# Performance work log

Hardware: AMD Instinct MI355X
Metric: run time of the kernel (lower is better)

## Reference

```python
import jax, jax.numpy as jnp
import numpy as np

N, D, H, E = 4_194_304, 8, 16, 2  # tokens, d_model, d_hidden, num_expert


def setup_inputs() -> dict:
    key = jax.random.key(0)
    ks = jax.random.split(key, 11)
    def w(k, shape, fan_in):
        return (jax.random.normal(k, shape, jnp.float32) / np.sqrt(fan_in)).astype(jnp.float32)
    return {
        "inp": jax.random.normal(ks[0], (N, D), jnp.float32),
        # non-MoE MLP: Linear(8,16) -> ReLU -> Linear(16,8)
        "W_a": w(ks[1], (D, H), D), "b_a": jnp.zeros((H,), jnp.float32),
        "W_b": w(ks[2], (H, D), H), "b_b": jnp.zeros((D,), jnp.float32),
        # NaiveGate: Linear(d_model, num_expert)
        "Wg": w(ks[3], (D, E), D), "bg": jnp.zeros((E,), jnp.float32),
        # per-expert MLP weights: d_model -> d_hidden -> d_model
        "We1": w(ks[4], (E, D, H), D), "be1": jnp.zeros((E, H), jnp.float32),
        "We2": w(ks[5], (E, H, D), H), "be2": jnp.zeros((E, D), jnp.float32),
    }


def reference(inp, W_a, b_a, W_b, b_b, Wg, bg, We1, be1, We2, be2):
    # non-MoE block: Linear -> ReLU -> Linear
    x = jnp.maximum(inp @ W_a + b_a, 0.0) @ W_b + b_b            # [N, D]
    # NaiveGate, top_k=1: argmax expert; softmax over a single score == 1.0
    logits = x @ Wg + bg                                         # [N, E]
    idx = jnp.argmax(logits, axis=-1)                            # [N]
    onehot = jax.nn.one_hot(idx, logits.shape[-1], dtype=x.dtype)  # [N, E]
    # expert MLPs computed densely for all E=2 experts, then top-1 select
    h = jax.nn.gelu(jnp.einsum('nd,edh->neh', x, We1) + be1, approximate=False)  # [N, E, H]
    y = jnp.einsum('neh,ehd->ned', h, We2) + be2                 # [N, E, D]
    out = jnp.einsum('ned,ne->nd', y, onehot)                    # [N, D]
    return jnp.sum(out)
```

## Files before the change

### kernel.cpp

```cpp
#include <hip/hip_runtime.h>
#include <math.h>

#define BLOCKS  4096
#define THREADS 256
#define NWAVES  (BLOCKS * THREADS / 64)
#define STEP    (NWAVES * 64)

typedef __attribute__((ext_vector_type(8))) short bf16x8;
typedef __attribute__((ext_vector_type(4))) float f32x4;
typedef __attribute__((ext_vector_type(2))) int   iv2;

union BF8 { unsigned u[4]; bf16x8 v; };

__device__ __forceinline__ unsigned cvt_pk_bf16(float lo, float hi)
{
    unsigned r;
    asm("v_cvt_pk_bf16_f32 %0, %1, %2" : "=v"(r) : "v"(lo), "v"(hi));
    return r;
}

__device__ __forceinline__ float gelu_fast(float x)
{
    const float e = __expf(-1.702f * x);
    return x * __builtin_amdgcn_rcpf(1.0f + e);
}

__global__ void moe_prep(const float* __restrict__ Wb,  const float* __restrict__ bb,
                         const float* __restrict__ Wg,  const float* __restrict__ bg,
                         const float* __restrict__ We1, const float* __restrict__ be1,
                         const float* __restrict__ We2, const float* __restrict__ be2,
                         float* __restrict__ wsc)
{
    const int t = threadIdx.x;
    if (t < 16) {
        float s = 0.f;
        #pragma unroll
        for (int d = 0; d < 8; ++d)
            s += Wb[t * 8 + d] * (Wg[d * 2 + 1] - Wg[d * 2 + 0]);
        wsc[t] = s;
    }
    if (t == 16) {
        float s = bg[1] - bg[0];
        #pragma unroll
        for (int d = 0; d < 8; ++d) s += bb[d] * (Wg[d * 2 + 1] - Wg[d * 2 + 0]);
        wsc[16] = s;
    }
    if (t == 17 || t == 18) {
        const int e = t - 17;
        float s = 0.f;
        #pragma unroll
        for (int d = 0; d < 8; ++d) s += be2[e * 8 + d];
        wsc[t] = s;
    }
    if (t >= 32 && t < 64) {
        const int e = (t - 32) >> 4, h = t & 15;
        float s = be1[e * 16 + h];
        #pragma unroll
        for (int d = 0; d < 8; ++d) s += bb[d] * We1[e * 128 + d * 16 + h];
        wsc[t] = s;
    }
    if (t >= 64 && t < 96) {
        const int e = (t - 64) >> 4, h = t & 15;
        float s = 0.f;
        #pragma unroll
        for (int d = 0; d < 8; ++d) s += We2[(e * 16 + h) * 8 + d];
        wsc[t] = s;
    }
    if (t >= 128 && t < 640) {
        const int idx = t - 128;
        const int e = idx >> 8, f = (idx >> 4) & 15, h = idx & 15;
        float s = 0.f;
        #pragma unroll
        for (int d = 0; d < 8; ++d) s += Wb[f * 8 + d] * We1[e * 128 + d * 16 + h];
        wsc[128 + idx] = s;
    }
}

__global__ void __launch_bounds__(THREADS, 4)
moe_main(const float* __restrict__ inp,
         const float* __restrict__ Wa, const float* __restrict__ ba,
         const float* __restrict__ wsc,
         float* __restrict__ blocksums, int ntok)
{
    __shared__ float wavered[4];
    const int t  = threadIdx.x;
    const int l  = t & 63;
    const int lg = l >> 4;
    const int lr = l & 15;
    const bool lo16 = (l < 16);
    const bool lo32 = (l < 32);

    BF8 aWa, aM0, aM1;
    #pragma unroll
    for (int j2 = 0; j2 < 4; ++j2) {
        const float w0 = lo16 ? Wa[(2 * j2) * 16 + lr]     : 0.f;
        const float w1 = lo16 ? Wa[(2 * j2 + 1) * 16 + lr] : 0.f;
        aWa.u[j2] = cvt_pk_bf16(w0, w1);
        const int f0 = 8 * lg + 2 * j2;
        const float m00 = lo32 ? wsc[128 + f0 * 16 + lr]       : 0.f;
        const float m01 = lo32 ? wsc[128 + (f0 + 1) * 16 + lr] : 0.f;
        aM0.u[j2] = cvt_pk_bf16(m00, m01);
        const float m10 = lo32 ? wsc[384 + f0 * 16 + lr]       : 0.f;
        const float m11 = lo32 ? wsc[384 + (f0 + 1) * 16 + lr] : 0.f;
        aM1.u[j2] = cvt_pk_bf16(m10, m11);
    }

    f32x4 cba, ccb0, ccb1, vwg, vs20, vs21;
    #pragma unroll
    for (int r = 0; r < 4; ++r) {
        const int h = lg * 4 + r;
        cba[r]  = ba[h];
        vwg[r]  = wsc[h];
        ccb0[r] = wsc[32 + h];
        ccb1[r] = wsc[48 + h];
        vs20[r] = wsc[64 + h];
        vs21[r] = wsc[80 + h];
    }
    const float cg4  = wsc[16] * 0.25f;
    const float sbq0 = wsc[17] * 0.25f;
    const float sbq1 = wsc[18] * 0.25f;

    int addrB[4];
    #pragma unroll
    for (int j = 0; j < 4; ++j)
        addrB[j] = ((lg * 2 + (j >> 1)) * 16 + lr) * 4;

    const int gwave = (blockIdx.x * THREADS + t) >> 6;
    const float4* __restrict__ p4 = (const float4*)inp;
    float local = 0.f;

    const int niter = ntok / STEP;
    int tok = gwave * 64 + l;
    float4 a0 = p4[2 * tok];
    float4 a1 = p4[2 * tok + 1];

    for (int it = 0; it < niter; ++it) {
        const float4 c0 = a0;
        const float4 c1 = a1;
        if (it + 1 < niter) {
            a0 = p4[2 * (tok + STEP)];
            a1 = p4[2 * (tok + STEP) + 1];
        }
        tok += STEP;

        unsigned pin[4];
        pin[0] = cvt_pk_bf16(c0.x, c0.y);
        pin[1] = cvt_pk_bf16(c0.z, c0.w);
        pin[2] = cvt_pk_bf16(c1.x, c1.y);
        pin[3] = cvt_pk_bf16(c1.z, c1.w);

        #pragma unroll
        for (int m = 0; m < 4; ++m) {
            const int srcA = m * 64 + lr * 4;
            BF8 bin;
            #pragma unroll
            for (int j = 0; j < 4; ++j)
                bin.u[j] = (unsigned)__builtin_amdgcn_ds_bpermute(srcA, (int)pin[j]);

            const f32x4 C = __builtin_amdgcn_mfma_f32_16x16x32_bf16(
                                aWa.v, bin.v, cba, 0, 0, 0);
            f32x4 rh;
            #pragma unroll
            for (int r = 0; r < 4; ++r) rh[r] = fmaxf(C[r], 0.f);

            float pg = cg4;
            #pragma unroll
            for (int r = 0; r < 4; ++r) pg = fmaf(rh[r], vwg[r], pg);
            const iv2 gs = __builtin_amdgcn_permlane32_swap(
                               __float_as_int(pg), __float_as_int(pg),
                               false, false);
            float pg32 = __int_as_float(gs.x) + __int_as_float(gs.y);
            pg32 += __shfl_xor(pg32, 16);
            const bool sel = pg32 > 0.f;

            const unsigned pr0 = cvt_pk_bf16(rh[0], rh[1]);
            const unsigned pr1 = cvt_pk_bf16(rh[2], rh[3]);
            BF8 bb2;
            #pragma unroll
            for (int j = 0; j < 4; ++j)
                bb2.u[j] = (unsigned)__builtin_amdgcn_ds_bpermute(
                               addrB[j], (int)((j & 1) ? pr1 : pr0));

            const f32x4 C0 = __builtin_amdgcn_mfma_f32_16x16x32_bf16(
                                 aM0.v, bb2.v, ccb0, 0, 0, 0);
            const f32x4 C1 = __builtin_amdgcn_mfma_f32_16x16x32_bf16(
                                 aM1.v, bb2.v, ccb1, 0, 0, 0);

            #pragma unroll
            for (int r = 0; r < 4; ++r) {
                const float pre = sel ? C1[r] : C0[r];
                const float g   = gelu_fast(pre);
                const float s2  = sel ? vs21[r] : vs20[r];
                local = fmaf(g, s2, local);
            }
            local += sel ? sbq1 : sbq0;
        }
    }

    #pragma unroll
    for (int off = 32; off > 0; off >>= 1)
        local += __shfl_down(local, off);
    if ((t & 63) == 0) wavered[t >> 6] = local;
    __syncthreads();
    if (t == 0)
        blocksums[blockIdx.x] = wavered[0] + wavered[1] + wavered[2] + wavered[3];
}

__global__ void __launch_bounds__(256)
moe_reduce(const float* __restrict__ blocksums, float* __restrict__ out)
{
    __shared__ float wavered[4];
    float v = 0.f;
    for (int i = threadIdx.x; i < BLOCKS; i += 256) v += blocksums[i];
    #pragma unroll
    for (int off = 32; off > 0; off >>= 1)
        v += __shfl_down(v, off);
    if ((threadIdx.x & 63) == 0) wavered[threadIdx.x >> 6] = v;
    __syncthreads();
    if (threadIdx.x == 0)
        out[0] = wavered[0] + wavered[1] + wavered[2] + wavered[3];
}

extern "C" void kernel_launch(void* const* d_in, const int* in_sizes, int n_in,
                              void* d_out, int out_size, void* d_ws, size_t ws_size,
                              hipStream_t stream)
{
    const float* inp = (const float*)d_in[0];
    const float* Wa  = (const float*)d_in[1];
    const float* ba  = (const float*)d_in[2];
    const float* Wb  = (const float*)d_in[3];
    const float* bb  = (const float*)d_in[4];
    const float* Wg  = (const float*)d_in[5];
    const float* bg  = (const float*)d_in[6];
    const float* We1 = (const float*)d_in[7];
    const float* be1 = (const float*)d_in[8];
    const float* We2 = (const float*)d_in[9];
    const float* be2 = (const float*)d_in[10];

    const int ntok = in_sizes[0] / 8;

    float* wsc       = (float*)d_ws;
    float* blocksums = (float*)d_ws + 640;
    float* out       = (float*)d_out;

    hipLaunchKernelGGL(moe_prep, dim3(1), dim3(640), 0, stream,
                       Wb, bb, Wg, bg, We1, be1, We2, be2, wsc);
    hipLaunchKernelGGL(moe_main, dim3(BLOCKS), dim3(THREADS), 0, stream,
                       inp, Wa, ba, wsc, blocksums, ntok);
    hipLaunchKernelGGL(moe_reduce, dim3(1), dim3(256), 0, stream,
                       blocksums, out);
}
```

Before: 56.37 us.

## Replace grid-stride prefetch loop with one token per thread over larger grid

Launches four times as many blocks so each thread processes a single token, removing the grid-stride loop and its register double-buffered prefetch. This aims to rely on hardware wave scheduling for latency hiding instead of explicit prefetch. In exchange, every block repeats the weight/constant setup, the final reduction kernel sums more partials, and the kernel now assumes the token count equals the grid size exactly.

```diff
diff --git a/kernel.cpp b/kernel.cpp
--- a/kernel.cpp
+++ b/kernel.cpp
@@ -1,16 +1,17 @@
 #include <hip/hip_runtime.h>
 #include <math.h>
 
-#define BLOCKS  4096
+#define BLOCKS  16384
 #define THREADS 256
-#define NWAVES  (BLOCKS * THREADS / 64)
-#define STEP    (NWAVES * 64)
 
 typedef __attribute__((ext_vector_type(8))) short bf16x8;
 typedef __attribute__((ext_vector_type(4))) float f32x4;
 typedef __attribute__((ext_vector_type(2))) int   iv2;
 
 union BF8 { unsigned u[4]; bf16x8 v; };
+
+__device__ __forceinline__ iv2 swap32(int a, int b)
+{ return __builtin_amdgcn_permlane32_swap(a, b, false, false); }
 
 __device__ __forceinline__ unsigned cvt_pk_bf16(float lo, float hi)
 {
@@ -80,7 +81,7 @@
 moe_main(const float* __restrict__ inp,
          const float* __restrict__ Wa, const float* __restrict__ ba,
          const float* __restrict__ wsc,
-         float* __restrict__ blocksums, int ntok)
+         float* __restrict__ blocksums)
 {
     __shared__ float wavered[4];
     const int t  = threadIdx.x;
@@ -120,81 +121,65 @@
     const float sbq0 = wsc[17] * 0.25f;
     const float sbq1 = wsc[18] * 0.25f;
 
-    int addrB[4];
-    #pragma unroll
-    for (int j = 0; j < 4; ++j)
-        addrB[j] = ((lg * 2 + (j >> 1)) * 16 + lr) * 4;
-
     const int gwave = (blockIdx.x * THREADS + t) >> 6;
+    const int tok   = gwave * 64 + l;
     const float4* __restrict__ p4 = (const float4*)inp;
+    const float4 c0 = p4[2 * tok];
+    const float4 c1 = p4[2 * tok + 1];
+
+    unsigned pin[4];
+    pin[0] = cvt_pk_bf16(c0.x, c0.y);
+    pin[1] = cvt_pk_bf16(c0.z, c0.w);
+    pin[2] = cvt_pk_bf16(c1.x, c1.y);
+    pin[3] = cvt_pk_bf16(c1.z, c1.w);
+
     float local = 0.f;
 
-    const int niter = ntok / STEP;
-    int tok = gwave * 64 + l;
-    float4 a0 = p4[2 * tok];
-    float4 a1 = p4[2 * tok + 1];
-
-    for (int it = 0; it < niter; ++it) {
-        const float4 c0 = a0;
-        const float4 c1 = a1;
-        if (it + 1 < niter) {
-            a0 = p4[2 * (tok + STEP)];
-            a1 = p4[2 * (tok + STEP) + 1];
+    #pragma unroll
+    for (int m = 0; m < 4; ++m) {
+        const int srcA = m * 64 + lr * 4;
+        BF8 bin;
+        #pragma unroll
+        for (int j = 0; j < 4; ++j)
+            bin.u[j] = (unsigned)__builtin_amdgcn_ds_bpermute(srcA, (int)pin[j]);
+
+        const f32x4 C = __builtin_amdgcn_mfma_f32_16x16x32_bf16(
+                            aWa.v, bin.v, cba, 0, 0, 0);
+        f32x4 rh;
+        #pragma unroll
+        for (int r = 0; r < 4; ++r) rh[r] = fmaxf(C[r], 0.f);
+
+        float pg = cg4;
+        #pragma unroll
+        for (int r = 0; r < 4; ++r) pg = fmaf(rh[r], vwg[r], pg);
+        const iv2 gs = swap32(__float_as_int(pg), __float_as_int(pg));
+        float pg32 = __int_as_float(gs.x) + __int_as_float(gs.y);
+        pg32 += __shfl_xor(pg32, 16);
+        const bool sel = pg32 > 0.f;
+
+        const unsigned pr0 = cvt_pk_bf16(rh[0], rh[1]);
+        const unsigned pr1 = cvt_pk_bf16(rh[2], rh[3]);
+        BF8 b2;
+        #pragma unroll
+        for (int j = 0; j < 4; ++j) {
+            const int addr = ((lg * 2 + (j >> 1)) * 16 + lr) * 4;
+            b2.u[j] = (unsigned)__builtin_amdgcn_ds_bpermute(
+                          addr, (int)((j & 1) ? pr1 : pr0));
         }
-        tok += STEP;
-
-        unsigned pin[4];
-        pin[0] = cvt_pk_bf16(c0.x, c0.y);
-        pin[1] = cvt_pk_bf16(c0.z, c0.w);
-        pin[2] = cvt_pk_bf16(c1.x, c1.y);
-        pin[3] = cvt_pk_bf16(c1.z, c1.w);
-
-        #pragma unroll
-        for (int m = 0; m < 4; ++m) {
-            const int srcA = m * 64 + lr * 4;
-            BF8 bin;
-            #pragma unroll
-            for (int j = 0; j < 4; ++j)
-                bin.u[j] = (unsigned)__builtin_amdgcn_ds_bpermute(srcA, (int)pin[j]);
-
-            const f32x4 C = __builtin_amdgcn_mfma_f32_16x16x32_bf16(
-                                aWa.v, bin.v, cba, 0, 0, 0);
-            f32x4 rh;
-            #pragma unroll
-            for (int r = 0; r < 4; ++r) rh[r] = fmaxf(C[r], 0.f);
-
-            float pg = cg4;
-            #pragma unroll
-            for (int r = 0; r < 4; ++r) pg = fmaf(rh[r], vwg[r], pg);
-            const iv2 gs = __builtin_amdgcn_permlane32_swap(
-                               __float_as_int(pg), __float_as_int(pg),
-                               false, false);
-            float pg32 = __int_as_float(gs.x) + __int_as_float(gs.y);
-            pg32 += __shfl_xor(pg32, 16);
-            const bool sel = pg32 > 0.f;
-
-            const unsigned pr0 = cvt_pk_bf16(rh[0], rh[1]);
-            const unsigned pr1 = cvt_pk_bf16(rh[2], rh[3]);
-            BF8 bb2;
-            #pragma unroll
-            for (int j = 0; j < 4; ++j)
-                bb2.u[j] = (unsigned)__builtin_amdgcn_ds_bpermute(
-                               addrB[j], (int)((j & 1) ? pr1 : pr0));
-
-            const f32x4 C0 = __builtin_amdgcn_mfma_f32_16x16x32_bf16(
-                                 aM0.v, bb2.v, ccb0, 0, 0, 0);
-            const f32x4 C1 = __builtin_amdgcn_mfma_f32_16x16x32_bf16(
-                                 aM1.v, bb2.v, ccb1, 0, 0, 0);
-
-            #pragma unroll
-            for (int r = 0; r < 4; ++r) {
-                const float pre = sel ? C1[r] : C0[r];
-                const float g   = gelu_fast(pre);
-                const float s2  = sel ? vs21[r] : vs20[r];
-                local = fmaf(g, s2, local);
-            }
-            local += sel ? sbq1 : sbq0;
+
+        const f32x4 C0 = __builtin_amdgcn_mfma_f32_16x16x32_bf16(
+                             aM0.v, b2.v, ccb0, 0, 0, 0);
+        const f32x4 C1 = __builtin_amdgcn_mfma_f32_16x16x32_bf16(
+                             aM1.v, b2.v, ccb1, 0, 0, 0);
+
+        #pragma unroll
+        for (int r = 0; r < 4; ++r) {
+            const float pre = sel ? C1[r] : C0[r];
+            const float g   = gelu_fast(pre);
+            const float s2  = sel ? vs21[r] : vs20[r];
+            local = fmaf(g, s2, local);
         }
+        local += sel ? sbq1 : sbq0;
     }
 
     #pragma unroll
@@ -237,8 +222,6 @@
     const float* We2 = (const float*)d_in[9];
     const float* be2 = (const float*)d_in[10];
 
-    const int ntok = in_sizes[0] / 8;
-
     float* wsc       = (float*)d_ws;
     float* blocksums = (float*)d_ws + 640;
     float* out       = (float*)d_out;
@@ -246,7 +229,7 @@
     hipLaunchKernelGGL(moe_prep, dim3(1), dim3(640), 0, stream,
                        Wb, bb, Wg, bg, We1, be1, We2, be2, wsc);
     hipLaunchKernelGGL(moe_main, dim3(BLOCKS), dim3(THREADS), 0, stream,
-                       inp, Wa, ba, wsc, blocksums, ntok);
+                       inp, Wa, ba, wsc, blocksums);
     hipLaunchKernelGGL(moe_reduce, dim3(1), dim3(256), 0, stream,
                        blocksums, out);
 }
```

After: 78.06 us. 1.38x slower.
